# Kernel tuning notes

Measured on AMD Instinct MI355X. Metric: run time of the kernel, lower is better.

## Reference

```python
import jax, jax.numpy as jnp
import numpy as np

N, E, D, H = 50000, 400000, 128, 4
NEG_SLOPE = 0.2
LN_EPS = 1e-5


def setup_inputs() -> dict:
    key = jax.random.key(0)
    ks = jax.random.split(key, 16)
    s = 1.0 / np.sqrt(D)
    inp = {
        'x': jax.random.normal(ks[0], (N, D), jnp.float32),
        'edge_index': jax.random.randint(ks[1], (2, E), 0, N, jnp.int32),
        # GATv2Conv params: lin_l/lin_r: Linear(D, H*D), att: [H, D], bias: [D] (concat=False)
        'Wl': jax.random.normal(ks[2], (H * D, D), jnp.float32) * s,
        'bl': jnp.zeros((H * D,), jnp.float32),
        'Wr': jax.random.normal(ks[3], (H * D, D), jnp.float32) * s,
        'br': jnp.zeros((H * D,), jnp.float32),
        'att': jax.random.normal(ks[4], (H, D), jnp.float32) * s,
        'bias': jnp.zeros((D,), jnp.float32),
        # LayerNorm 1
        'g1': jnp.ones((D,), jnp.float32), 'be1': jnp.zeros((D,), jnp.float32),
        # FFN: Linear(D, 2D) -> GELU -> Linear(2D, D)
        'W1': jax.random.normal(ks[5], (2 * D, D), jnp.float32) * s,
        'b1': jnp.zeros((2 * D,), jnp.float32),
        'W2': jax.random.normal(ks[6], (D, 2 * D), jnp.float32) * (1.0 / np.sqrt(2 * D)),
        'b2': jnp.zeros((D,), jnp.float32),
        # LayerNorm 2
        'g2': jnp.ones((D,), jnp.float32), 'be2': jnp.zeros((D,), jnp.float32),
    }
    return inp


def _layernorm(x, g, b):
    mu = jnp.mean(x, -1, keepdims=True)
    var = jnp.mean(jnp.square(x - mu), -1, keepdims=True)
    return (x - mu) * jax.lax.rsqrt(var + LN_EPS) * g + b


def _gatv2(x, edge_index, Wl, bl, Wr, br, att, bias):
    # Self-loops (PyG default add_self_loops=True)
    loop = jnp.arange(N, dtype=edge_index.dtype)
    src = jnp.concatenate([edge_index[0], loop])  # [E+N]
    dst = jnp.concatenate([edge_index[1], loop])
    xl = (x @ Wl.T + bl).reshape(N, H, D)  # source transform
    xr = (x @ Wr.T + br).reshape(N, H, D)  # target transform
    m = xl[src] + xr[dst]                  # [E+N, H, D]
    e = jnp.einsum('ehd,hd->eh', jax.nn.leaky_relu(m, NEG_SLOPE), att)
    # segment softmax over destination nodes
    emax = jax.ops.segment_max(e, dst, num_segments=N)
    ee = jnp.exp(e - emax[dst])
    denom = jax.ops.segment_sum(ee, dst, num_segments=N)
    alpha = ee / (denom[dst] + 1e-16)      # [E+N, H]  (dropout=0.1 skipped: eval mode)
    out = jax.ops.segment_sum(xl[src] * alpha[:, :, None], dst, num_segments=N)
    return out.mean(axis=1) + bias         # concat=False -> head mean


def reference(x, edge_index, Wl, bl, Wr, br, att, bias, g1, be1, W1, b1, W2, b2, g2, be2):
    h = _gatv2(x, edge_index, Wl, bl, Wr, br, att, bias)
    x = _layernorm(x + h, g1, be1)
    h = jax.nn.gelu(x @ W1.T + b1, approximate=False) @ W2.T + b2
    x = _layernorm(x + h, g2, be2)
    return x
```

## Files before the change

### kernel.cpp

```cpp
#include <hip/hip_runtime.h>
#include <cstdint>
#include <cstddef>

#define N_NODES 50000
#define N_EDGES 400000
#define EN_TOT  (N_EDGES + N_NODES)
#define NC_SCAN ((N_NODES + 511) / 512)
#define NEG_SLOPE 0.2f
#define LN_EPS 1e-5f

typedef short bf16x8 __attribute__((ext_vector_type(8)));
typedef float f32x4  __attribute__((ext_vector_type(4)));

__device__ __forceinline__ ushort f2bf(float f) {
    union { float f; uint32_t u; } c; c.f = f;
    uint32_t u = c.u + 0x7FFFu + ((c.u >> 16) & 1u);
    return (ushort)(u >> 16);
}
__device__ __forceinline__ uint32_t pk2(float a, float b) {
    return (uint32_t)f2bf(a) | ((uint32_t)f2bf(b) << 16);
}
__device__ __forceinline__ float bf_lo(uint32_t u) {
    union { uint32_t u; float f; } c; c.u = u << 16; return c.f;
}
__device__ __forceinline__ float bf_hi(uint32_t u) {
    union { uint32_t u; float f; } c; c.u = u & 0xFFFF0000u; return c.f;
}
__device__ __forceinline__ float bfu(ushort v) {
    union { uint32_t u; float f; } c; c.u = ((uint32_t)v) << 16; return c.f;
}

__global__ __launch_bounds__(256) void prep(
    const float* __restrict__ Wl, const float* __restrict__ Wr,
    const float* __restrict__ W1, const float* __restrict__ W2,
    const float* __restrict__ att, ushort* __restrict__ wb,
    int* __restrict__ counts2 , int* __restrict__ state )
{
    int i = blockIdx.x * 256 + threadIdx.x;
    const float* src; int off;
    if (i < 65536)       { src = Wl;  off = i; }
    else if (i < 131072) { src = Wr;  off = i - 65536; }
    else if (i < 163840) { src = W1;  off = i - 131072; }
    else if (i < 196608) { src = W2;  off = i - 163840; }
    else                 { src = att; off = i - 196608; }
    wb[i] = f2bf(src[off]);
    if (i < 100000) counts2[i] = 0;
    if (i < 256)    state[i] = 0;
}

__global__ __launch_bounds__(256) void gemm_lr(
    const float* __restrict__ x, const ushort* __restrict__ wcat,
    const float* __restrict__ bl, const float* __restrict__ br,
    ushort* __restrict__ xlb, ushort* __restrict__ xrb,
    const int* __restrict__ dst, int* __restrict__ counts)
{
    __shared__ ushort As[128 * 128];
    __shared__ ushort Bs[128 * 136];
    const int tid  = threadIdx.x;
    const int rb   = blockIdx.x * 128;
    const int wave = tid >> 6, lane = tid & 63;
    const int wm   = (wave >> 1) * 64, wn = (wave & 1) * 64;
    const int lr   = lane & 15, lq = lane >> 4;

    {
        int e0 = blockIdx.x * 1152;
        int e1 = e0 + 1152; if (e1 > EN_TOT) e1 = EN_TOT;
        for (int e = e0 + tid; e < e1; e += 256) {
            int d = (e < N_EDGES) ? dst[e] : (e - N_EDGES);
            atomicAdd(counts + d, 1);
        }
    }

    #pragma unroll
    for (int i = 0; i < 8; ++i) {
        int chunk = tid + i * 256;
        int rr = chunk >> 4, cc = chunk & 15;
        int gr = rb + rr;
        float4 v0 = make_float4(0.f,0.f,0.f,0.f), v1 = v0;
        if (gr < N_NODES) {
            v0 = *(const float4*)(x + (size_t)gr * 128 + cc * 8);
            v1 = *(const float4*)(x + (size_t)gr * 128 + cc * 8 + 4);
        }
        uint4 h = make_uint4(pk2(v0.x,v0.y), pk2(v0.z,v0.w),
                             pk2(v1.x,v1.y), pk2(v1.z,v1.w));
        *(uint4*)(As + rr * 128 + ((cc ^ (rr & 15)) * 8)) = h;
    }

    for (int cbk = 0; cbk < 8; ++cbk) {
        __syncthreads();
        #pragma unroll
        for (int i = 0; i < 8; ++i) {
            int chunk = tid + i * 256;
            int rr = chunk >> 4, cc = chunk & 15;
            uint4 vb = *(const uint4*)(wcat + (size_t)(cbk * 128 + rr) * 128 + cc * 8);
            *(uint4*)(Bs + rr * 128 + ((cc ^ (rr & 15)) * 8)) = vb;
        }
        __syncthreads();

        f32x4 zero = {0.f,0.f,0.f,0.f};
        f32x4 acc[4][4];
        #pragma unroll
        for (int i = 0; i < 4; ++i)
            #pragma unroll
            for (int j = 0; j < 4; ++j) acc[i][j] = zero;

        #pragma unroll
        for (int q = 0; q < 4; ++q) {
            int csw = ((q * 4 + lq) ^ lr) * 8;
            bf16x8 bfr[4], af[4];
            #pragma unroll
            for (int i = 0; i < 4; ++i) {
                bfr[i] = *(const bf16x8*)(Bs + (wm + i * 16 + lr) * 128 + csw);
                af[i]  = *(const bf16x8*)(As + (wn + i * 16 + lr) * 128 + csw);
            }
            #pragma unroll
            for (int i = 0; i < 4; ++i)
                #pragma unroll
                for (int j = 0; j < 4; ++j)
                    acc[i][j] = __builtin_amdgcn_mfma_f32_16x16x32_bf16(
                        bfr[i], af[j], acc[i][j], 0, 0, 0);
        }

        __syncthreads();
        const float* bias = (cbk < 4) ? bl : br;
        ushort* outp = (cbk < 4) ? xlb : xrb;
        const int cloc = (cbk & 3) * 128;
        #pragma unroll
        for (int i = 0; i < 4; ++i) {
            int wc = wm + i * 16 + lq * 4;
            float4 bv = *(const float4*)(bias + cloc + wc);
            #pragma unroll
            for (int j = 0; j < 4; ++j) {
                int nl = wn + j * 16 + lr;
                ushort4 o;
                o.x = f2bf(acc[i][j][0] + bv.x);
                o.y = f2bf(acc[i][j][1] + bv.y);
                o.z = f2bf(acc[i][j][2] + bv.z);
                o.w = f2bf(acc[i][j][3] + bv.w);
                *(ushort4*)(Bs + nl * 136 + wc) = o;
            }
        }
        __syncthreads();
        #pragma unroll
        for (int i = 0; i < 8; ++i) {
            int chunk = tid + i * 256;
            int row = chunk >> 4, cc = chunk & 15;
            int node = rb + row;
            if (node < N_NODES) {
                uint4 v = *(const uint4*)(Bs + row * 136 + cc * 8);
                *(uint4*)(outp + (size_t)node * 512 + cloc + cc * 8) = v;
            }
        }
    }
}

__global__ __launch_bounds__(64) void scan_lb(const int* __restrict__ counts,
                                              int* __restrict__ offs,
                                              unsigned long long* __restrict__ state)
{
    const int b = blockIdx.x, lane = threadIdx.x;
    const int base = b * 512 + lane * 8;
    int cnt[8];
    int s = 0;
    #pragma unroll
    for (int k = 0; k < 8; ++k) {
        int idx = base + k;
        cnt[k] = (idx < N_NODES) ? counts[idx] : 0;
        s += cnt[k];
    }
    int inc = s;
    #pragma unroll
    for (int d = 1; d < 64; d <<= 1) {
        int t = __shfl_up(inc, d, 64);
        if (lane >= d) inc += t;
    }
    const int total = __shfl(inc, 63, 64);

    if (lane == 0) {
        unsigned long long pub = ((unsigned long long)(b == 0 ? 2u : 1u) << 32)
                               | (unsigned)total;
        atomicExch(&state[b], pub);
    }

    int prefix = 0;
    if (b > 0) {
        int p0 = b - 1;
        while (true) {
            int p = p0 - lane;
            int flag, val;
            if (p >= 0) {
                unsigned long long v;
                do { v = atomicAdd(&state[p], 0ULL); flag = (int)(v >> 32); }
                while (flag == 0);
                val = (int)(unsigned)v;
            } else { flag = 2; val = 0; }
            unsigned long long mask = __ballot(flag == 2);
            int L = mask ? (__ffsll(mask) - 1) : 64;
            int take = (lane <= L) ? val : 0;
            #pragma unroll
            for (int m = 32; m; m >>= 1) take += __shfl_xor(take, m, 64);
            prefix += take;
            if (L < 64) break;
            p0 -= 64;
        }
        if (lane == 0)
            atomicExch(&state[b], (2ULL << 32) | (unsigned)(prefix + total));
    }

    int run = prefix + inc - s;
    #pragma unroll
    for (int k = 0; k < 8; ++k) {
        int idx = base + k;
        if (idx < N_NODES) { offs[idx] = run; run += cnt[k]; }
    }
    if (b == NC_SCAN - 1 && lane == 63) offs[N_NODES] = prefix + inc;
}

__global__ __launch_bounds__(256) void scatter_edges(
    const int* __restrict__ src, const int* __restrict__ dst,
    const int* __restrict__ offs, int* __restrict__ cursor,
    int* __restrict__ srcList)
{
    int i = blockIdx.x * 256 + threadIdx.x;
    if (i >= EN_TOT) return;
    int s, d;
    if (i < N_EDGES) { s = src[i]; d = dst[i]; }
    else             { s = d = i - N_EDGES; }
    int pos = atomicAdd(cursor + d, 1);
    srcList[offs[d] + pos] = s;
}

__global__ __launch_bounds__(256) void gat_fused(
    const float* __restrict__ x, const ushort* __restrict__ xl,
    const ushort* __restrict__ xr, const int* __restrict__ offs,
    const int* __restrict__ srcList, const ushort* __restrict__ attb,
    const float* __restrict__ bias, const float* __restrict__ g1,
    const float* __restrict__ be1, ushort* __restrict__ x1b)
{
    const int wave = threadIdx.x >> 6;
    const int lane = threadIdx.x & 63;
    const int v = blockIdx.x * 4 + wave;
    if (v >= N_NODES) return;

    uint4 rw = *(const uint4*)(xr + (size_t)v * 512 + lane * 8);
    uint4 aw = *(const uint4*)(attb + lane * 8);
    float r[8], at[8];
    r[0]=bf_lo(rw.x); r[1]=bf_hi(rw.x); r[2]=bf_lo(rw.y); r[3]=bf_hi(rw.y);
    r[4]=bf_lo(rw.z); r[5]=bf_hi(rw.z); r[6]=bf_lo(rw.w); r[7]=bf_hi(rw.w);
    at[0]=bf_lo(aw.x); at[1]=bf_hi(aw.x); at[2]=bf_lo(aw.y); at[3]=bf_hi(aw.y);
    at[4]=bf_lo(aw.z); at[5]=bf_hi(aw.z); at[6]=bf_lo(aw.w); at[7]=bf_hi(aw.w);

    float acc[8] = {0.f,0.f,0.f,0.f,0.f,0.f,0.f,0.f};
    float lh = 0.f;

    const int jb = offs[v], je = offs[v + 1];
    const int jlast = je - 1;
    auto LD = [&](int j) -> uint4 {
        int jj = (j < jlast) ? j : jlast;
        return *(const uint4*)(xl + (size_t)srcList[jj] * 512 + lane * 8);
    };
    uint4 q0 = LD(jb), q1 = LD(jb + 1), q2 = LD(jb + 2);
    for (int j = jb; j < je; ++j) {
        uint4 cur = q0; q0 = q1; q1 = q2; q2 = LD(j + 3);

        float b[8];
        b[0]=bf_lo(cur.x); b[1]=bf_hi(cur.x); b[2]=bf_lo(cur.y); b[3]=bf_hi(cur.y);
        b[4]=bf_lo(cur.z); b[5]=bf_hi(cur.z); b[6]=bf_lo(cur.w); b[7]=bf_hi(cur.w);
        float p = 0.f;
        #pragma unroll
        for (int k = 0; k < 8; ++k) {
            float s  = b[k] + r[k];
            float lr2 = fmaxf(s, 0.f) + NEG_SLOPE * fminf(s, 0.f);
            p = fmaf(lr2, at[k], p);
        }
        p += __shfl_xor(p, 1, 64);
        p += __shfl_xor(p, 2, 64);
        p += __shfl_xor(p, 4, 64);
        p += __shfl_xor(p, 8, 64);
        float w = __expf(p);
        lh += w;
        #pragma unroll
        for (int k = 0; k < 8; ++k) acc[k] = fmaf(w, b[k], acc[k]);
    }

    const float inv = 1.0f / lh;
    const int d0 = (lane & 15) * 8;
    const size_t xo = (size_t)v * 128 + d0;

    float4 xv0 = *(const float4*)(x + xo);
    float4 xv1 = *(const float4*)(x + xo + 4);
    float4 bb0 = *(const float4*)(bias + d0);
    float4 bb1 = *(const float4*)(bias + d0 + 4);
    float xr8[8] = {xv0.x,xv0.y,xv0.z,xv0.w,xv1.x,xv1.y,xv1.z,xv1.w};
    float bi8[8] = {bb0.x,bb0.y,bb0.z,bb0.w,bb1.x,bb1.y,bb1.z,bb1.w};

    float y[8];
    float s = 0.f;
    #pragma unroll
    for (int k = 0; k < 8; ++k) {
        float o = acc[k] * inv;
        o += __shfl_xor(o, 16, 64);
        o += __shfl_xor(o, 32, 64);
        float yy = xr8[k] + o * 0.25f + bi8[k];
        y[k] = yy;
        s += yy;
    }
    s += __shfl_xor(s, 1, 64);
    s += __shfl_xor(s, 2, 64);
    s += __shfl_xor(s, 4, 64);
    s += __shfl_xor(s, 8, 64);
    float mu = s * (1.0f / 128.0f);
    float ss = 0.f;
    #pragma unroll
    for (int k = 0; k < 8; ++k) { float d = y[k] - mu; ss += d * d; }
    ss += __shfl_xor(ss, 1, 64);
    ss += __shfl_xor(ss, 2, 64);
    ss += __shfl_xor(ss, 4, 64);
    ss += __shfl_xor(ss, 8, 64);
    float rs = rsqrtf(ss * (1.0f / 128.0f) + LN_EPS);

    if ((lane >> 4) == 0) {
        float4 g0 = *(const float4*)(g1 + d0);
        float4 g4 = *(const float4*)(g1 + d0 + 4);
        float4 e0 = *(const float4*)(be1 + d0);
        float4 e4 = *(const float4*)(be1 + d0 + 4);
        float gg[8] = {g0.x,g0.y,g0.z,g0.w,g4.x,g4.y,g4.z,g4.w};
        float ee[8] = {e0.x,e0.y,e0.z,e0.w,e4.x,e4.y,e4.z,e4.w};
        float z[8];
        #pragma unroll
        for (int k = 0; k < 8; ++k) z[k] = (y[k] - mu) * rs * gg[k] + ee[k];
        ushort4 zb0, zb1;
        zb0.x=f2bf(z[0]); zb0.y=f2bf(z[1]); zb0.z=f2bf(z[2]); zb0.w=f2bf(z[3]);
        zb1.x=f2bf(z[4]); zb1.y=f2bf(z[5]); zb1.z=f2bf(z[6]); zb1.w=f2bf(z[7]);
        *(ushort4*)(x1b + xo)     = zb0;
        *(ushort4*)(x1b + xo + 4) = zb1;
    }
}

__global__ __launch_bounds__(256) void ffn_fused(
    const ushort* __restrict__ x1b, const ushort* __restrict__ w1b,
    const float* __restrict__ b1, const ushort* __restrict__ w2b,
    const float* __restrict__ b2, const float* __restrict__ g2,
    const float* __restrict__ be2, float* __restrict__ out)
{
    __shared__ ushort As[128 * 128];
    __shared__ ushort Bs[128 * 128];
    __shared__ ushort Ts[128 * 128];
    const int tid  = threadIdx.x;
    const int rb   = blockIdx.x * 128;
    const int wave = tid >> 6, lane = tid & 63;
    const int wm   = (wave >> 1) * 64, wn = (wave & 1) * 64;
    const int lr   = lane & 15, lq = lane >> 4;

    #pragma unroll
    for (int i = 0; i < 8; ++i) {
        int chunk = tid + i * 256;
        int rr = chunk >> 4, cc = chunk & 15;
        int gr = rb + rr;
        uint4 va = make_uint4(0u,0u,0u,0u);
        if (gr < N_NODES) va = *(const uint4*)(x1b + (size_t)gr * 128 + cc * 8);
        *(uint4*)(As + rr * 128 + ((cc ^ (rr & 15)) * 8)) = va;
    }

    f32x4 zero = {0.f,0.f,0.f,0.f};
    f32x4 acc2[4][4];
    #pragma unroll
    for (int i = 0; i < 4; ++i)
        #pragma unroll
        for (int j = 0; j < 4; ++j) acc2[i][j] = zero;

    for (int half = 0; half < 2; ++half) {
        __syncthreads();
        #pragma unroll
        for (int i = 0; i < 8; ++i) {
            int chunk = tid + i * 256;
            int rr = chunk >> 4, cc = chunk & 15;
            uint4 vb = *(const uint4*)(w1b + (size_t)(half * 128 + rr) * 128 + cc * 8);
            *(uint4*)(Bs + rr * 128 + ((cc ^ (rr & 15)) * 8)) = vb;
        }
        __syncthreads();

        f32x4 acc1[4][4];
        #pragma unroll
        for (int i = 0; i < 4; ++i)
            #pragma unroll
            for (int j = 0; j < 4; ++j) acc1[i][j] = zero;

        #pragma unroll
        for (int q = 0; q < 4; ++q) {
            int csw = ((q * 4 + lq) ^ lr) * 8;
            bf16x8 bfr[4], af[4];
            #pragma unroll
            for (int i = 0; i < 4; ++i) {
                bfr[i] = *(const bf16x8*)(Bs + (wm + i * 16 + lr) * 128 + csw);
                af[i]  = *(const bf16x8*)(As + (wn + i * 16 + lr) * 128 + csw);
            }
            #pragma unroll
            for (int i = 0; i < 4; ++i)
                #pragma unroll
                for (int j = 0; j < 4; ++j)
                    acc1[i][j] = __builtin_amdgcn_mfma_f32_16x16x32_bf16(
                        bfr[i], af[j], acc1[i][j], 0, 0, 0);
        }

        #pragma unroll
        for (int i = 0; i < 4; ++i) {
            int wc = wm + i * 16 + lq * 4;
            float4 bv = *(const float4*)(b1 + half * 128 + wc);
            #pragma unroll
            for (int j = 0; j < 4; ++j) {
                int nl = wn + j * 16 + lr;
                float v0 = acc1[i][j][0] + bv.x;
                float v1 = acc1[i][j][1] + bv.y;
                float v2 = acc1[i][j][2] + bv.z;
                float v3 = acc1[i][j][3] + bv.w;
                v0 = v0 * 0.5f * (1.0f + erff(v0 * 0.70710678118654752f));
                v1 = v1 * 0.5f * (1.0f + erff(v1 * 0.70710678118654752f));
                v2 = v2 * 0.5f * (1.0f + erff(v2 * 0.70710678118654752f));
                v3 = v3 * 0.5f * (1.0f + erff(v3 * 0.70710678118654752f));
                ushort4 o;
                o.x = f2bf(v0); o.y = f2bf(v1); o.z = f2bf(v2); o.w = f2bf(v3);
                int sw = (((wc >> 3) ^ (nl & 15)) * 8) + (wc & 7);
                *(ushort4*)(Ts + nl * 128 + sw) = o;
            }
        }
        __syncthreads();
        #pragma unroll
        for (int i = 0; i < 8; ++i) {
            int chunk = tid + i * 256;
            int rr = chunk >> 4, cc = chunk & 15;
            uint4 vb = *(const uint4*)(w2b + (size_t)rr * 256 + half * 128 + cc * 8);
            *(uint4*)(Bs + rr * 128 + ((cc ^ (rr & 15)) * 8)) = vb;
        }
        __syncthreads();

        #pragma unroll
        for (int q = 0; q < 4; ++q) {
            int csw = ((q * 4 + lq) ^ lr) * 8;
            bf16x8 bfr[4], af[4];
            #pragma unroll
            for (int i = 0; i < 4; ++i) {
                bfr[i] = *(const bf16x8*)(Bs + (wm + i * 16 + lr) * 128 + csw);
                af[i]  = *(const bf16x8*)(Ts + (wn + i * 16 + lr) * 128 + csw);
            }
            #pragma unroll
            for (int i = 0; i < 4; ++i)
                #pragma unroll
                for (int j = 0; j < 4; ++j)
                    acc2[i][j] = __builtin_amdgcn_mfma_f32_16x16x32_bf16(
                        bfr[i], af[j], acc2[i][j], 0, 0, 0);
        }
    }

    __syncthreads();
    float* sums = (float*)Ts;
    float* ssqs = (float*)(Ts + 2048);

    #pragma unroll
    for (int j = 0; j < 4; ++j) {
        int nl = wn + j * 16 + lr;
        float s = 0.f, q2 = 0.f;
        #pragma unroll
        for (int i = 0; i < 4; ++i) {
            int wc = wm + i * 16 + lq * 4;
            float4 bv = *(const float4*)(b2 + wc);
            const ushort* ap = As + nl * 128 + (((wc >> 3) ^ (nl & 15)) * 8) + (wc & 7);
            float y0 = acc2[i][j][0] + bv.x + bfu(ap[0]);
            float y1 = acc2[i][j][1] + bv.y + bfu(ap[1]);
            float y2 = acc2[i][j][2] + bv.z + bfu(ap[2]);
            float y3 = acc2[i][j][3] + bv.w + bfu(ap[3]);
            acc2[i][j][0] = y0; acc2[i][j][1] = y1;
            acc2[i][j][2] = y2; acc2[i][j][3] = y3;
            s  += y0 + y1 + y2 + y3;
            q2 += y0*y0 + y1*y1 + y2*y2 + y3*y3;
        }
        s  += __shfl_xor(s, 16, 64);  s  += __shfl_xor(s, 32, 64);
        q2 += __shfl_xor(q2, 16, 64); q2 += __shfl_xor(q2, 32, 64);
        if (lq == 0) {
            int half = wm >> 6;
            sums[half * 128 + nl] = s;
            ssqs[half * 128 + nl] = q2;
        }
    }
    __syncthreads();

    #pragma unroll
    for (int j = 0; j < 4; ++j) {
        int nl = wn + j * 16 + lr;
        int node = rb + nl;
        if (node >= N_NODES) continue;
        float tot = sums[nl] + sums[128 + nl];
        float tq  = ssqs[nl] + ssqs[128 + nl];
        float mu  = tot * (1.0f / 128.0f);
        float var = tq * (1.0f / 128.0f) - mu * mu;
        float rs  = rsqrtf(var + LN_EPS);
        #pragma unroll
        for (int i = 0; i < 4; ++i) {
            int wc = wm + i * 16 + lq * 4;
            float4 gv = *(const float4*)(g2 + wc);
            float4 ev = *(const float4*)(be2 + wc);
            float4 o;
            o.x = (acc2[i][j][0] - mu) * rs * gv.x + ev.x;
            o.y = (acc2[i][j][1] - mu) * rs * gv.y + ev.y;
            o.z = (acc2[i][j][2] - mu) * rs * gv.z + ev.z;
            o.w = (acc2[i][j][3] - mu) * rs * gv.w + ev.w;
            *(float4*)(out + (size_t)node * 128 + wc) = o;
        }
    }
}

extern "C" void kernel_launch(void* const* d_in, const int* in_sizes, int n_in,
                              void* d_out, int out_size, void* d_ws, size_t ws_size,
                              hipStream_t stream)
{
    const float* x    = (const float*)d_in[0];
    const int*   ei   = (const int*)  d_in[1];
    const float* Wl   = (const float*)d_in[2];
    const float* bl   = (const float*)d_in[3];
    const float* Wr   = (const float*)d_in[4];
    const float* br   = (const float*)d_in[5];
    const float* att  = (const float*)d_in[6];
    const float* bias = (const float*)d_in[7];
    const float* g1   = (const float*)d_in[8];
    const float* be1  = (const float*)d_in[9];
    const float* W1   = (const float*)d_in[10];
    const float* b1   = (const float*)d_in[11];
    const float* W2   = (const float*)d_in[12];
    const float* b2   = (const float*)d_in[13];
    const float* g2   = (const float*)d_in[14];
    const float* be2  = (const float*)d_in[15];
    float* out = (float*)d_out;

    char* ws = (char*)d_ws;
    size_t off = 0;
    auto alloc = [&](size_t bytes) -> void* {
        void* p = ws + off;
        off = (off + bytes + 255) & ~(size_t)255;
        return p;
    };
    ushort* xlb  = (ushort*)alloc((size_t)N_NODES * 512 * 2);
    ushort* xrb  = (ushort*)alloc((size_t)N_NODES * 512 * 2);
    ushort* x1b  = (ushort*)alloc((size_t)N_NODES * 128 * 2);
    ushort* wb   = (ushort*)alloc((size_t)197120 * 2);
    int*   offs    = (int*)alloc((size_t)(N_NODES + 1) * 4);
    int*   counts  = (int*)alloc((size_t)N_NODES * 4 * 2);
    int*   cursor  = counts + N_NODES;
    unsigned long long* state = (unsigned long long*)alloc(256 * 4);
    int*   srcList = (int*)alloc((size_t)EN_TOT * 4);

    ushort* wcat = wb;
    ushort* w1b  = wb + 131072;
    ushort* w2b  = wb + 163840;
    ushort* attb = wb + 196608;

    prep<<<770, 256, 0, stream>>>(Wl, Wr, W1, W2, att, wb, counts, (int*)state);

    gemm_lr<<<391, 256, 0, stream>>>(x, wcat, bl, br, xlb, xrb,
                                     ei + N_EDGES, counts);

    scan_lb<<<NC_SCAN, 64, 0, stream>>>(counts, offs, state);
    scatter_edges<<<(EN_TOT + 255) / 256, 256, 0, stream>>>(ei, ei + N_EDGES,
                                                           offs, cursor, srcList);

    gat_fused<<<12500, 256, 0, stream>>>(x, xlb, xrb, offs, srcList, attb,
                                         bias, g1, be1, x1b);

    ffn_fused<<<391, 256, 0, stream>>>(x1b, w1b, b1, w2b, b2, g2, be2, out);
}
```

Baseline: 303.8 us.

## Switch intermediates from bf16 to fp16 and use packed-half math in GAT aggregation

Replaces bf16 storage and MFMA with fp16 throughout (weights, xl/xr, activations), and uses hardware packed conversion (cvt_pkrtz) in place of manual bit rounding. The GAT edge loop now runs in packed half2 arithmetic: leaky-relu via max, attention dot via fdot2, and weighted accumulation in fp16. The source index is made wave-uniform with readfirstlane, and the three-deep prefetch becomes a one-ahead prefetch. This aims to cut ALU work in the gather loop and the conversion cost. It risks fp16 overflow and precision loss, since unnormalised exp weights are accumulated in half, and the shallower prefetch may expose memory latency.

```diff
diff --git a/kernel.cpp b/kernel.cpp
--- a/kernel.cpp
+++ b/kernel.cpp
@@ -6,28 +6,26 @@
 #define N_EDGES 400000
 #define EN_TOT  (N_EDGES + N_NODES)
 #define NC_SCAN ((N_NODES + 511) / 512)
-#define NEG_SLOPE 0.2f
 #define LN_EPS 1e-5f
 
-typedef short bf16x8 __attribute__((ext_vector_type(8)));
-typedef float f32x4  __attribute__((ext_vector_type(4)));
-
-__device__ __forceinline__ ushort f2bf(float f) {
-    union { float f; uint32_t u; } c; c.f = f;
-    uint32_t u = c.u + 0x7FFFu + ((c.u >> 16) & 1u);
-    return (ushort)(u >> 16);
-}
-__device__ __forceinline__ uint32_t pk2(float a, float b) {
-    return (uint32_t)f2bf(a) | ((uint32_t)f2bf(b) << 16);
-}
-__device__ __forceinline__ float bf_lo(uint32_t u) {
-    union { uint32_t u; float f; } c; c.u = u << 16; return c.f;
-}
-__device__ __forceinline__ float bf_hi(uint32_t u) {
-    union { uint32_t u; float f; } c; c.u = u & 0xFFFF0000u; return c.f;
-}
-__device__ __forceinline__ float bfu(ushort v) {
-    union { uint32_t u; float f; } c; c.u = ((uint32_t)v) << 16; return c.f;
+typedef _Float16 h2    __attribute__((ext_vector_type(2)));
+typedef __fp16   g2t   __attribute__((ext_vector_type(2)));
+typedef _Float16 f16x8 __attribute__((ext_vector_type(8)));
+typedef float    f32x4 __attribute__((ext_vector_type(4)));
+
+__device__ __forceinline__ uint32_t pkh(float a, float b) {
+    g2t t = __builtin_amdgcn_cvt_pkrtz(a, b);
+    union { g2t h; uint32_t u; } c; c.h = t; return c.u;
+}
+__device__ __forceinline__ h2 as_h2(uint32_t u) {
+    union { uint32_t u; h2 h; } c; c.u = u; return c.h;
+}
+__device__ __forceinline__ float fdot2(h2 a, h2 b, float c) {
+    union { h2 h; g2t g; } ca, cb; ca.h = a; cb.h = b;
+    return __builtin_amdgcn_fdot2(ca.g, cb.g, c, false);
+}
+__device__ __forceinline__ float hfu(ushort v) {
+    union { ushort u; _Float16 h; } c; c.u = v; return (float)c.h;
 }
 
 __global__ __launch_bounds__(256) void prep(
@@ -43,7 +41,8 @@
     else if (i < 163840) { src = W1;  off = i - 131072; }
     else if (i < 196608) { src = W2;  off = i - 163840; }
     else                 { src = att; off = i - 196608; }
-    wb[i] = f2bf(src[off]);
+    union { _Float16 h; ushort u; } c; c.h = (_Float16)src[off];
+    wb[i] = c.u;
     if (i < 100000) counts2[i] = 0;
     if (i < 256)    state[i] = 0;
 }
@@ -81,8 +80,8 @@
             v0 = *(const float4*)(x + (size_t)gr * 128 + cc * 8);
             v1 = *(const float4*)(x + (size_t)gr * 128 + cc * 8 + 4);
         }
-        uint4 h = make_uint4(pk2(v0.x,v0.y), pk2(v0.z,v0.w),
-                             pk2(v1.x,v1.y), pk2(v1.z,v1.w));
+        uint4 h = make_uint4(pkh(v0.x,v0.y), pkh(v0.z,v0.w),
+                             pkh(v1.x,v1.y), pkh(v1.z,v1.w));
         *(uint4*)(As + rr * 128 + ((cc ^ (rr & 15)) * 8)) = h;
     }
 
@@ -107,17 +106,17 @@
         #pragma unroll
         for (int q = 0; q < 4; ++q) {
             int csw = ((q * 4 + lq) ^ lr) * 8;
-            bf16x8 bfr[4], af[4];
+            f16x8 bfr[4], af[4];
             #pragma unroll
             for (int i = 0; i < 4; ++i) {
-                bfr[i] = *(const bf16x8*)(Bs + (wm + i * 16 + lr) * 128 + csw);
-                af[i]  = *(const bf16x8*)(As + (wn + i * 16 + lr) * 128 + csw);
+                bfr[i] = *(const f16x8*)(Bs + (wm + i * 16 + lr) * 128 + csw);
+                af[i]  = *(const f16x8*)(As + (wn + i * 16 + lr) * 128 + csw);
             }
             #pragma unroll
             for (int i = 0; i < 4; ++i)
                 #pragma unroll
                 for (int j = 0; j < 4; ++j)
-                    acc[i][j] = __builtin_amdgcn_mfma_f32_16x16x32_bf16(
+                    acc[i][j] = __builtin_amdgcn_mfma_f32_16x16x32_f16(
                         bfr[i], af[j], acc[i][j], 0, 0, 0);
         }
 
@@ -132,12 +131,10 @@
             #pragma unroll
             for (int j = 0; j < 4; ++j) {
                 int nl = wn + j * 16 + lr;
-                ushort4 o;
-                o.x = f2bf(acc[i][j][0] + bv.x);
-                o.y = f2bf(acc[i][j][1] + bv.y);
-                o.z = f2bf(acc[i][j][2] + bv.z);
-                o.w = f2bf(acc[i][j][3] + bv.w);
-                *(ushort4*)(Bs + nl * 136 + wc) = o;
+                uint2 o;
+                o.x = pkh(acc[i][j][0] + bv.x, acc[i][j][1] + bv.y);
+                o.y = pkh(acc[i][j][2] + bv.z, acc[i][j][3] + bv.w);
+                *(uint2*)(Bs + nl * 136 + wc) = o;
             }
         }
         __syncthreads();
@@ -244,46 +241,50 @@
 
     uint4 rw = *(const uint4*)(xr + (size_t)v * 512 + lane * 8);
     uint4 aw = *(const uint4*)(attb + lane * 8);
-    float r[8], at[8];
-    r[0]=bf_lo(rw.x); r[1]=bf_hi(rw.x); r[2]=bf_lo(rw.y); r[3]=bf_hi(rw.y);
-    r[4]=bf_lo(rw.z); r[5]=bf_hi(rw.z); r[6]=bf_lo(rw.w); r[7]=bf_hi(rw.w);
-    at[0]=bf_lo(aw.x); at[1]=bf_hi(aw.x); at[2]=bf_lo(aw.y); at[3]=bf_hi(aw.y);
-    at[4]=bf_lo(aw.z); at[5]=bf_hi(aw.z); at[6]=bf_lo(aw.w); at[7]=bf_hi(aw.w);
-
-    float acc[8] = {0.f,0.f,0.f,0.f,0.f,0.f,0.f,0.f};
+    h2 r0 = as_h2(rw.x), r1 = as_h2(rw.y), r2 = as_h2(rw.z), r3 = as_h2(rw.w);
+    h2 a0 = as_h2(aw.x), a1 = as_h2(aw.y), a2 = as_h2(aw.z), a3 = as_h2(aw.w);
+    const h2 k02 = {(_Float16)0.2f, (_Float16)0.2f};
+
+    h2 acc0 = {0, 0}, acc1 = {0, 0}, acc2 = {0, 0}, acc3 = {0, 0};
     float lh = 0.f;
 
     const int jb = offs[v], je = offs[v + 1];
-    const int jlast = je - 1;
-    auto LD = [&](int j) -> uint4 {
-        int jj = (j < jlast) ? j : jlast;
-        return *(const uint4*)(xl + (size_t)srcList[jj] * 512 + lane * 8);
-    };
-    uint4 q0 = LD(jb), q1 = LD(jb + 1), q2 = LD(jb + 2);
+    int u = __builtin_amdgcn_readfirstlane(srcList[jb]);
+    uint4 cur = *(const uint4*)(xl + (size_t)u * 512 + lane * 8);
     for (int j = jb; j < je; ++j) {
-        uint4 cur = q0; q0 = q1; q1 = q2; q2 = LD(j + 3);
-
-        float b[8];
-        b[0]=bf_lo(cur.x); b[1]=bf_hi(cur.x); b[2]=bf_lo(cur.y); b[3]=bf_hi(cur.y);
-        b[4]=bf_lo(cur.z); b[5]=bf_hi(cur.z); b[6]=bf_lo(cur.w); b[7]=bf_hi(cur.w);
+        int jn = (j + 1 < je) ? (j + 1) : j;
+        int un = __builtin_amdgcn_readfirstlane(srcList[jn]);
+        uint4 nxt = *(const uint4*)(xl + (size_t)un * 512 + lane * 8);
+
+        h2 b0 = as_h2(cur.x), b1 = as_h2(cur.y), b2 = as_h2(cur.z), b3 = as_h2(cur.w);
+        h2 s0 = b0 + r0, s1 = b1 + r1, s2 = b2 + r2, s3 = b3 + r3;
+        h2 l0 = __builtin_elementwise_max(s0, s0 * k02);
+        h2 l1 = __builtin_elementwise_max(s1, s1 * k02);
+        h2 l2 = __builtin_elementwise_max(s2, s2 * k02);
+        h2 l3 = __builtin_elementwise_max(s3, s3 * k02);
         float p = 0.f;
-        #pragma unroll
-        for (int k = 0; k < 8; ++k) {
-            float s  = b[k] + r[k];
-            float lr2 = fmaxf(s, 0.f) + NEG_SLOPE * fminf(s, 0.f);
-            p = fmaf(lr2, at[k], p);
-        }
+        p = fdot2(l0, a0, p);
+        p = fdot2(l1, a1, p);
+        p = fdot2(l2, a2, p);
+        p = fdot2(l3, a3, p);
         p += __shfl_xor(p, 1, 64);
         p += __shfl_xor(p, 2, 64);
         p += __shfl_xor(p, 4, 64);
         p += __shfl_xor(p, 8, 64);
         float w = __expf(p);
         lh += w;
-        #pragma unroll
-        for (int k = 0; k < 8; ++k) acc[k] = fmaf(w, b[k], acc[k]);
+        h2 wh = as_h2(pkh(w, w));
+        acc0 += wh * b0;
+        acc1 += wh * b1;
+        acc2 += wh * b2;
+        acc3 += wh * b3;
+        cur = nxt;
     }
 
     const float inv = 1.0f / lh;
+    float o8[8] = {(float)acc0[0], (float)acc0[1], (float)acc1[0], (float)acc1[1],
+                   (float)acc2[0], (float)acc2[1], (float)acc3[0], (float)acc3[1]};
+
     const int d0 = (lane & 15) * 8;
     const size_t xo = (size_t)v * 128 + d0;
 
@@ -298,7 +299,7 @@
     float s = 0.f;
     #pragma unroll
     for (int k = 0; k < 8; ++k) {
-        float o = acc[k] * inv;
+        float o = o8[k] * inv;
         o += __shfl_xor(o, 16, 64);
         o += __shfl_xor(o, 32, 64);
         float yy = xr8[k] + o * 0.25f + bi8[k];
@@ -329,11 +330,11 @@
         float z[8];
         #pragma unroll
         for (int k = 0; k < 8; ++k) z[k] = (y[k] - mu) * rs * gg[k] + ee[k];
-        ushort4 zb0, zb1;
-        zb0.x=f2bf(z[0]); zb0.y=f2bf(z[1]); zb0.z=f2bf(z[2]); zb0.w=f2bf(z[3]);
-        zb1.x=f2bf(z[4]); zb1.y=f2bf(z[5]); zb1.z=f2bf(z[6]); zb1.w=f2bf(z[7]);
-        *(ushort4*)(x1b + xo)     = zb0;
-        *(ushort4*)(x1b + xo + 4) = zb1;
+        uint2 z0, z1;
+        z0.x = pkh(z[0], z[1]); z0.y = pkh(z[2], z[3]);
+        z1.x = pkh(z[4], z[5]); z1.y = pkh(z[6], z[7]);
+        *(uint2*)(x1b + xo)     = z0;
+        *(uint2*)(x1b + xo + 4) = z1;
     }
 }
 
@@ -389,17 +390,17 @@
         #pragma unroll
         for (int q = 0; q < 4; ++q) {
             int csw = ((q * 4 + lq) ^ lr) * 8;
-            bf16x8 bfr[4], af[4];
+            f16x8 bfr[4], af[4];
             #pragma unroll
             for (int i = 0; i < 4; ++i) {
-                bfr[i] = *(const bf16x8*)(Bs + (wm + i * 16 + lr) * 128 + csw);
-                af[i]  = *(const bf16x8*)(As + (wn + i * 16 + lr) * 128 + csw);
+                bfr[i] = *(const f16x8*)(Bs + (wm + i * 16 + lr) * 128 + csw);
+                af[i]  = *(const f16x8*)(As + (wn + i * 16 + lr) * 128 + csw);
             }
             #pragma unroll
             for (int i = 0; i < 4; ++i)
                 #pragma unroll
                 for (int j = 0; j < 4; ++j)
-                    acc1[i][j] = __builtin_amdgcn_mfma_f32_16x16x32_bf16(
+                    acc1[i][j] = __builtin_amdgcn_mfma_f32_16x16x32_f16(
                         bfr[i], af[j], acc1[i][j], 0, 0, 0);
         }
 
@@ -418,10 +419,10 @@
                 v1 = v1 * 0.5f * (1.0f + erff(v1 * 0.70710678118654752f));
                 v2 = v2 * 0.5f * (1.0f + erff(v2 * 0.70710678118654752f));
                 v3 = v3 * 0.5f * (1.0f + erff(v3 * 0.70710678118654752f));
-                ushort4 o;
-                o.x = f2bf(v0); o.y = f2bf(v1); o.z = f2bf(v2); o.w = f2bf(v3);
+                uint2 o;
+                o.x = pkh(v0, v1); o.y = pkh(v2, v3);
                 int sw = (((wc >> 3) ^ (nl & 15)) * 8) + (wc & 7);
-                *(ushort4*)(Ts + nl * 128 + sw) = o;
+                *(uint2*)(Ts + nl * 128 + sw) = o;
             }
         }
         __syncthreads();
@@ -437,17 +438,17 @@
         #pragma unroll
         for (int q = 0; q < 4; ++q) {
             int csw = ((q * 4 + lq) ^ lr) * 8;
-            bf16x8 bfr[4], af[4];
+            f16x8 bfr[4], af[4];
             #pragma unroll
             for (int i = 0; i < 4; ++i) {
-                bfr[i] = *(const bf16x8*)(Bs + (wm + i * 16 + lr) * 128 + csw);
-                af[i]  = *(const bf16x8*)(Ts + (wn + i * 16 + lr) * 128 + csw);
+                bfr[i] = *(const f16x8*)(Bs + (wm + i * 16 + lr) * 128 + csw);
+                af[i]  = *(const f16x8*)(Ts + (wn + i * 16 + lr) * 128 + csw);
             }
             #pragma unroll
             for (int i = 0; i < 4; ++i)
                 #pragma unroll
                 for (int j = 0; j < 4; ++j)
-                    acc2[i][j] = __builtin_amdgcn_mfma_f32_16x16x32_bf16(
+                    acc2[i][j] = __builtin_amdgcn_mfma_f32_16x16x32_f16(
                         bfr[i], af[j], acc2[i][j], 0, 0, 0);
         }
     }
@@ -465,10 +466,10 @@
             int wc = wm + i * 16 + lq * 4;
             float4 bv = *(const float4*)(b2 + wc);
             const ushort* ap = As + nl * 128 + (((wc >> 3) ^ (nl & 15)) * 8) + (wc & 7);
-            float y0 = acc2[i][j][0] + bv.x + bfu(ap[0]);
-            float y1 = acc2[i][j][1] + bv.y + bfu(ap[1]);
-            float y2 = acc2[i][j][2] + bv.z + bfu(ap[2]);
-            float y3 = acc2[i][j][3] + bv.w + bfu(ap[3]);
+            float y0 = acc2[i][j][0] + bv.x + hfu(ap[0]);
+            float y1 = acc2[i][j][1] + bv.y + hfu(ap[1]);
+            float y2 = acc2[i][j][2] + bv.z + hfu(ap[2]);
+            float y3 = acc2[i][j][3] + bv.w + hfu(ap[3]);
             acc2[i][j][0] = y0; acc2[i][j][1] = y1;
             acc2[i][j][2] = y2; acc2[i][j][3] = y3;
             s  += y0 + y1 + y2 + y3;
```

New measurement: 302.0 us. No clear change (-0.6%).
